# Kernel optimization log

Hardware: AMD Instinct MI355X
Metric: run time of the kernel (lower is better)

Reference implementation:

```python
import jax, jax.numpy as jnp
import numpy as np

H, B, S, E, V, C = 1024, 1024, 128, 6, 3, 10


def setup_inputs() -> dict:
    key = jax.random.key(0)
    ks = jax.random.split(key, 18)
    sH = 1.0 / np.sqrt(H)

    def n(k, shape, scale):
        return (jax.random.normal(k, shape, dtype=jnp.float32) * scale)

    return {
        'x': jax.random.randint(ks[0], (B, S), 0, V),
        'emb': n(ks[1], (V, E), 1.0),
        'W_gx': n(ks[2], (H, E), 1.0 / np.sqrt(E)),
        'W_gh': n(ks[3], (H, H), sH),
        'b_g': n(ks[4], (H, 1), sH),
        'W_ix': n(ks[5], (H, E), 1.0 / np.sqrt(E)),
        'W_ih': n(ks[6], (H, H), sH),
        'b_i': n(ks[7], (H, 1), sH),
        'W_fx': n(ks[8], (H, E), 1.0 / np.sqrt(E)),
        'W_fh': n(ks[9], (H, H), sH),
        'b_f': n(ks[10], (H, 1), sH),
        'W_ox': n(ks[11], (H, E), 1.0 / np.sqrt(E)),
        'W_oh': n(ks[12], (H, H), sH),
        'b_o': n(ks[13], (H, 1), sH),
        'W_ph': n(ks[14], (C, H), sH),
        'b_p': n(ks[15], (C, 1), sH),
        'h_init': n(ks[16], (H, B), 1.0),
        'c_init': n(ks[17], (H, B), 1.0),
    }


def reference(x, emb, W_gx, W_gh, b_g, W_ix, W_ih, b_i, W_fx, W_fh, b_f,
              W_ox, W_oh, b_o, W_ph, b_p, h_init, c_init):
    T = x.shape[1] - 1  # torch loop runs over seq_length - 1 steps
    e = emb[x[:, :T]]  # [B, T, E]
    # Precompute all input-to-gate projections in one batched contraction each.
    Xg = jnp.einsum('he,bte->thb', W_gx, e)  # [T, H, B]
    Xi = jnp.einsum('he,bte->thb', W_ix, e)
    Xf = jnp.einsum('he,bte->thb', W_fx, e)
    Xo = jnp.einsum('he,bte->thb', W_ox, e)

    def step(carry, xs):
        h, c = carry  # [H, B]
        xg, xi, xf, xo = xs
        g = jnp.tanh(xg + W_gh @ h + b_g)
        i = jax.nn.sigmoid(xi + W_ih @ h + b_i)
        f = jax.nn.sigmoid(xf + W_fh @ h + b_f)
        o = jax.nn.sigmoid(xo + W_oh @ h + b_o)
        c2 = g * i + c * f
        h2 = jnp.tanh(c2) * o
        return (h2, c2), None

    (h, c), _ = jax.lax.scan(step, (h_init, c_init), (Xg, Xi, Xf, Xo))
    p = W_ph @ h + b_p  # [C, B]
    return jax.nn.log_softmax(p.T, axis=-1)  # [B, C]
```

## Files before the change

kernel.cpp:

```cpp
#include <hip/hip_runtime.h>

constexpr int kH = 1024;
constexpr int kB = 1024;
constexpr int kS = 128;
constexpr int kT = 127;
constexpr int kE = 6;
constexpr int kV = 3;
constexpr int kC = 10;

typedef short s16x8 __attribute__((ext_vector_type(8)));
typedef short s16x4 __attribute__((ext_vector_type(4)));
typedef float f32x4 __attribute__((ext_vector_type(4)));
typedef unsigned short u16;

__device__ __forceinline__ float b2f(u16 u) {
    return __uint_as_float(((unsigned)u) << 16);
}
__device__ __forceinline__ u16 f2b(float f) {
    unsigned u = __float_as_uint(f);
    return (u16)((u + 0x7FFFu + ((u >> 16) & 1u)) >> 16);
}
__device__ __forceinline__ float sigmoid_fast(float x) {
    return 1.0f / (1.0f + __expf(-x));
}
__device__ __forceinline__ float tanh_fast(float x) {
    return 2.0f / (1.0f + __expf(-2.0f * x)) - 1.0f;
}
__device__ __forceinline__ float clamp30(float x) {
    return fminf(fmaxf(x, -30.0f), 30.0f);
}

__device__ __forceinline__ void async_copy16(const u16* g, u16* l) {
    __builtin_amdgcn_global_load_lds(
        (const __attribute__((address_space(1))) void*)g,
        (__attribute__((address_space(3))) void*)l, 16, 0, 0);
}

__global__ __launch_bounds__(256) void prep_weights(
    const float* __restrict__ Wgh, const float* __restrict__ Wih,
    const float* __restrict__ Wfh, const float* __restrict__ Woh,
    u16* __restrict__ wsw)
{
    unsigned grp = blockIdx.x * 256 + threadIdx.x;
    const int lane = grp & 63;
    const int lm   = lane & 15;
    const int quad = lane >> 4;
    const int k0   = (grp >> 6) & 7;
    const int g    = (grp >> 9) & 3;
    const int kc   = (grp >> 11) & 3;
    const int by   = grp >> 13;
    const float* src = (g == 0) ? Wgh : (g == 1) ? Wih : (g == 2) ? Wfh : Woh;
    const int row = by * 16 + lm;
    const int k   = kc * 256 + k0 * 32 + quad * 8;
    f32x4 v0 = *(const f32x4*)(src + (size_t)row * kH + k);
    f32x4 v1 = *(const f32x4*)(src + (size_t)row * kH + k + 4);
    s16x8 o;
#pragma unroll
    for (int j = 0; j < 4; ++j) o[j] = (short)f2b(v0[j]);
#pragma unroll
    for (int j = 0; j < 4; ++j) o[4 + j] = (short)f2b(v1[j]);
    *(s16x8*)(wsw + (size_t)grp * 8) = o;
}

__global__ __launch_bounds__(1024) void prep_hc(
    const float* __restrict__ h0, const float* __restrict__ c0,
    u16* __restrict__ hA, float* __restrict__ cT)
{
    __shared__ float th[32][33];
    __shared__ float tc[32][33];
    int b = blockIdx.x * 32 + threadIdx.x;
    int h = blockIdx.y * 32 + threadIdx.y;
    th[threadIdx.y][threadIdx.x] = h0[(size_t)h * kB + b];
    tc[threadIdx.y][threadIdx.x] = c0[(size_t)h * kB + b];
    __syncthreads();
    int ob = blockIdx.x * 32 + threadIdx.y;
    int oh = blockIdx.y * 32 + threadIdx.x;
    hA[(size_t)ob * kH + oh] = f2b(th[threadIdx.x][threadIdx.y]);
    cT[(size_t)ob * kH + oh] = tc[threadIdx.x][threadIdx.y];
}

__global__ __launch_bounds__(256) void prep_q(
    const float* __restrict__ Wgx, const float* __restrict__ Wix,
    const float* __restrict__ Wfx, const float* __restrict__ Wox,
    const float* __restrict__ bg,  const float* __restrict__ bi,
    const float* __restrict__ bf_, const float* __restrict__ bo,
    const float* __restrict__ emb, float* __restrict__ Q)
{
    int tid = blockIdx.x * blockDim.x + threadIdx.x;
    if (tid >= 4 * kH) return;
    int g = tid >> 10;
    int h = tid & (kH - 1);
    const float* Wx = (g == 0) ? Wgx : (g == 1) ? Wix : (g == 2) ? Wfx : Wox;
    const float* bb = (g == 0) ? bg  : (g == 1) ? bi  : (g == 2) ? bf_ : bo;
    float w[kE];
#pragma unroll
    for (int e = 0; e < kE; ++e) w[e] = Wx[h * kE + e];
#pragma unroll
    for (int v = 0; v < kV; ++v) {
        float s = bb[h];
#pragma unroll
        for (int e = 0; e < kE; ++e) s += w[e] * emb[v * kE + e];
        Q[tid * 4 + v] = s;
    }
    Q[tid * 4 + 3] = 0.0f;
}

__global__ __launch_bounds__(256, 2) void lstm_step(
    const u16* __restrict__ wsw, const float* __restrict__ Q,
    const int* __restrict__ x, int t,
    const short* __restrict__ hin, u16* __restrict__ hout,
    float* __restrict__ cT)
{
    __shared__ u16 wlds[2][16384];

    const int tid  = threadIdx.x;
    const int lane = tid & 63;
    const int wave = tid >> 6;
    const int lm   = lane & 15;
    const int quad = lane >> 4;
    const int blk  = blockIdx.x;
    const int xcd  = blk & 7;
    const int slot = blk >> 3;
    const int by   = xcd * 8 + (slot & 7);
    const int bx   = slot >> 3;
    const int r0 = by * 16;
    const int c0 = bx * 128 + wave * 32;

    const u16* wswblk = wsw + (size_t)by * 65536;

    f32x4 acc[4][2];
    const f32x4 zero = {0.f, 0.f, 0.f, 0.f};
#pragma unroll
    for (int g = 0; g < 4; ++g)
#pragma unroll
        for (int n = 0; n < 2; ++n) acc[g][n] = zero;

    const int koff = quad * 8;
    const short* hrow0 = hin + (size_t)(c0 + lm) * kH + koff;
    const short* hrow1 = hin + (size_t)(c0 + 16 + lm) * kH + koff;

    {
        const u16* gsrc = wswblk;
#pragma unroll
        for (int rr = 0; rr < 8; ++rr) {
            const int ub = wave * 4096 + rr * 512;
            async_copy16(gsrc + ub + lane * 8, &wlds[0][ub]);
        }
        asm volatile("s_waitcnt vmcnt(0)" ::: "memory");
        __syncthreads();
    }

    s16x8 b0c = *(const s16x8*)(hrow0);
    s16x8 b1c = *(const s16x8*)(hrow1);

#pragma unroll 1
    for (int kc = 0; kc < 4; ++kc) {
        const int cur = kc & 1;
        if (kc < 3) {
            const u16* gsrc = wswblk + (size_t)(kc + 1) * 16384;
#pragma unroll
            for (int rr = 0; rr < 8; ++rr) {
                const int ub = wave * 4096 + rr * 512;
                async_copy16(gsrc + ub + lane * 8, &wlds[cur ^ 1][ub]);
            }
        }
#pragma unroll
        for (int k0 = 0; k0 < 8; ++k0) {
            s16x8 b0n = {0,0,0,0,0,0,0,0}, b1n = {0,0,0,0,0,0,0,0};
            const int nk = kc * 256 + (k0 + 1) * 32;
            if (nk < kH) {
                b0n = *(const s16x8*)(hrow0 + nk);
                b1n = *(const s16x8*)(hrow1 + nk);
            }
#pragma unroll
            for (int g = 0; g < 4; ++g) {
                const int f = ((g * 8 + k0) * 64 + lane) * 8;
                s16x8 a = *(const s16x8*)&wlds[cur][f];
                acc[g][0] = __builtin_amdgcn_mfma_f32_16x16x32_bf16(a, b0c, acc[g][0], 0, 0, 0);
                acc[g][1] = __builtin_amdgcn_mfma_f32_16x16x32_bf16(a, b1c, acc[g][1], 0, 0, 0);
            }
            b0c = b0n;
            b1c = b1n;
        }
        if (kc < 3) {
            asm volatile("s_waitcnt vmcnt(0)" ::: "memory");
            __syncthreads();
        }
    }

#pragma unroll
    for (int nt = 0; nt < 2; ++nt) {
        const int c = c0 + nt * 16 + lm;
        int v = x[c * kS + t];
        v = (v < 0) ? 0 : (v > kV - 1) ? (kV - 1) : v;
        const int rb = r0 + quad * 4;
        f32x4 cold = *(const f32x4*)(cT + (size_t)c * kH + rb);
        f32x4 cnew;
        s16x4 hnew;
#pragma unroll
        for (int reg = 0; reg < 4; ++reg) {
            const int r = rb + reg;
            float pg = clamp30(acc[0][nt][reg] + Q[(0 * kH + r) * 4 + v]);
            float pi = clamp30(acc[1][nt][reg] + Q[(1 * kH + r) * 4 + v]);
            float pf = clamp30(acc[2][nt][reg] + Q[(2 * kH + r) * 4 + v]);
            float po = clamp30(acc[3][nt][reg] + Q[(3 * kH + r) * 4 + v]);
            float gg = tanh_fast(pg);
            float ii = sigmoid_fast(pi);
            float ff = sigmoid_fast(pf);
            float oo = sigmoid_fast(po);
            float c2 = gg * ii + cold[reg] * ff;
            c2 = fminf(fmaxf(c2, -200.0f), 200.0f);
            cnew[reg] = c2;
            hnew[reg] = (short)f2b(tanh_fast(c2) * oo);
        }
        *(f32x4*)(cT + (size_t)c * kH + rb) = cnew;
        *(s16x4*)(hout + (size_t)c * kH + rb) = hnew;
    }
}

__global__ __launch_bounds__(256) void logits_kernel(
    const u16* __restrict__ hT, const float* __restrict__ Wph,
    const float* __restrict__ bp, float* __restrict__ out)
{
    const int wave = threadIdx.x >> 6;
    const int lane = threadIdx.x & 63;
    const int b = blockIdx.x * 4 + wave;

    const u16* hp = hT + (size_t)b * kH + lane * 16;
    float hf[16];
#pragma unroll
    for (int j = 0; j < 16; ++j) hf[j] = b2f(hp[j]);

    float p[kC];
#pragma unroll
    for (int cls = 0; cls < kC; ++cls) {
        const float* wp = Wph + (size_t)cls * kH + lane * 16;
        float s = 0.f;
#pragma unroll
        for (int j = 0; j < 16; ++j) s += hf[j] * wp[j];
#pragma unroll
        for (int off = 1; off < 64; off <<= 1) s += __shfl_xor(s, off, 64);
        p[cls] = fminf(fmaxf(s + bp[cls], -1.0e4f), 1.0e4f);
    }

    float m = p[0];
#pragma unroll
    for (int cls = 1; cls < kC; ++cls) m = fmaxf(m, p[cls]);
    float se = 0.f;
#pragma unroll
    for (int cls = 0; cls < kC; ++cls) se += __expf(p[cls] - m);
    float l = m + __logf(se);

    if (lane < kC) {
        float myp = p[0];
#pragma unroll
        for (int cls = 1; cls < kC; ++cls)
            if (lane == cls) myp = p[cls];
        out[(size_t)b * kC + lane] = myp - l;
    }
}

extern "C" void kernel_launch(void* const* d_in, const int* in_sizes, int n_in,
                              void* d_out, int out_size, void* d_ws, size_t ws_size,
                              hipStream_t stream)
{
    const int*   x   = (const int*)  d_in[0];
    const float* emb = (const float*)d_in[1];
    const float* Wgx = (const float*)d_in[2];
    const float* Wgh = (const float*)d_in[3];
    const float* bg  = (const float*)d_in[4];
    const float* Wix = (const float*)d_in[5];
    const float* Wih = (const float*)d_in[6];
    const float* bi  = (const float*)d_in[7];
    const float* Wfx = (const float*)d_in[8];
    const float* Wfh = (const float*)d_in[9];
    const float* bf_ = (const float*)d_in[10];
    const float* Wox = (const float*)d_in[11];
    const float* Woh = (const float*)d_in[12];
    const float* bo  = (const float*)d_in[13];
    const float* Wph = (const float*)d_in[14];
    const float* bp  = (const float*)d_in[15];
    const float* h0  = (const float*)d_in[16];
    const float* c0  = (const float*)d_in[17];

    char* ws = (char*)d_ws;
    float* Q   = (float*)ws;
    u16*   hA  = (u16*)(ws + (64 << 10));
    u16*   hB  = hA + (size_t)kB * kH;
    float* cT  = (float*)(hB + (size_t)kB * kH);
    u16*   wsw = (u16*)(cT + (size_t)kB * kH);

    prep_weights<<<dim3(2048), dim3(256), 0, stream>>>(Wgh, Wih, Wfh, Woh, wsw);
    prep_hc<<<dim3(kB / 32, kH / 32), dim3(32, 32), 0, stream>>>(h0, c0, hA, cT);
    prep_q<<<dim3(16), dim3(256), 0, stream>>>(Wgx, Wix, Wfx, Wox, bg, bi, bf_, bo, emb, Q);

    for (int t = 0; t < kT; ++t) {
        const u16* hin  = (t & 1) ? hB : hA;
        u16*       hout = (t & 1) ? hA : hB;
        lstm_step<<<dim3(512), dim3(256), 0, stream>>>(
            wsw, Q, x, t, (const short*)hin, hout, cT);
    }
    logits_kernel<<<dim3(kB / 4), dim3(256), 0, stream>>>(hB, Wph, bp, (float*)d_out);
}
```

Measured before the change: 2.936 ms.

## Replace per-step launches with persistent LSTM kernel using grid barriers

Replaces the 127 per-timestep kernel launches with one persistent kernel of 256 blocks that loops over time and synchronises through a two-level atomic grid barrier. The cell state now stays in registers, and 14 of the 32 K-slices of each block's weight slab stay resident in LDS, while the remaining slices are read from global/L2 each step. The input projection and the logits/log-softmax step are fused into the same kernel. This removes launch overhead and the repeated reloading of weights and cell state from memory. In exchange it depends on all 256 blocks being co-resident, and the spin barrier has a bounded timeout that could silently break ordering.

```diff
diff --git a/kernel.cpp b/kernel.cpp
--- a/kernel.cpp
+++ b/kernel.cpp
@@ -7,6 +7,7 @@
 constexpr int kE = 6;
 constexpr int kV = 3;
 constexpr int kC = 10;
+constexpr int kKL = 14;
 
 typedef short s16x8 __attribute__((ext_vector_type(8)));
 typedef short s16x4 __attribute__((ext_vector_type(4)));
@@ -39,19 +40,18 @@
 __global__ __launch_bounds__(256) void prep_weights(
     const float* __restrict__ Wgh, const float* __restrict__ Wih,
     const float* __restrict__ Wfh, const float* __restrict__ Woh,
-    u16* __restrict__ wsw)
+    short* __restrict__ wsw)
 {
     unsigned grp = blockIdx.x * 256 + threadIdx.x;
     const int lane = grp & 63;
     const int lm   = lane & 15;
     const int quad = lane >> 4;
-    const int k0   = (grp >> 6) & 7;
-    const int g    = (grp >> 9) & 3;
-    const int kc   = (grp >> 11) & 3;
+    const int g    = (grp >> 6) & 3;
+    const int k0   = (grp >> 8) & 31;
     const int by   = grp >> 13;
     const float* src = (g == 0) ? Wgh : (g == 1) ? Wih : (g == 2) ? Wfh : Woh;
     const int row = by * 16 + lm;
-    const int k   = kc * 256 + k0 * 32 + quad * 8;
+    const int k   = k0 * 32 + quad * 8;
     f32x4 v0 = *(const f32x4*)(src + (size_t)row * kH + k);
     f32x4 v1 = *(const f32x4*)(src + (size_t)row * kH + k + 4);
     s16x8 o;
@@ -62,56 +62,59 @@
     *(s16x8*)(wsw + (size_t)grp * 8) = o;
 }
 
-__global__ __launch_bounds__(1024) void prep_hc(
-    const float* __restrict__ h0, const float* __restrict__ c0,
-    u16* __restrict__ hA, float* __restrict__ cT)
+__global__ __launch_bounds__(1024) void prep_h(
+    const float* __restrict__ h0, u16* __restrict__ hA)
 {
     __shared__ float th[32][33];
-    __shared__ float tc[32][33];
     int b = blockIdx.x * 32 + threadIdx.x;
     int h = blockIdx.y * 32 + threadIdx.y;
     th[threadIdx.y][threadIdx.x] = h0[(size_t)h * kB + b];
-    tc[threadIdx.y][threadIdx.x] = c0[(size_t)h * kB + b];
     __syncthreads();
     int ob = blockIdx.x * 32 + threadIdx.y;
     int oh = blockIdx.y * 32 + threadIdx.x;
     hA[(size_t)ob * kH + oh] = f2b(th[threadIdx.x][threadIdx.y]);
-    cT[(size_t)ob * kH + oh] = tc[threadIdx.x][threadIdx.y];
-}
-
-__global__ __launch_bounds__(256) void prep_q(
+}
+
+__device__ __forceinline__ void gbar(unsigned* bar, int g, bool leader, int epoch) {
+    __threadfence();
+    __syncthreads();
+    if (threadIdx.x == 0) {
+        __hip_atomic_fetch_add(&bar[g * 32], 1u, __ATOMIC_RELEASE,
+                               __HIP_MEMORY_SCOPE_AGENT);
+        if (leader) {
+            const unsigned gt = 32u * (unsigned)epoch;
+            int gc = 0;
+            while (__hip_atomic_load(&bar[g * 32], __ATOMIC_ACQUIRE,
+                                     __HIP_MEMORY_SCOPE_AGENT) < gt)
+                if (++gc > (1 << 18)) break;
+            __hip_atomic_fetch_add(&bar[256], 1u, __ATOMIC_RELEASE,
+                                   __HIP_MEMORY_SCOPE_AGENT);
+        }
+        const unsigned t8 = 8u * (unsigned)epoch;
+        int gc = 0;
+        while (__hip_atomic_load(&bar[256], __ATOMIC_ACQUIRE,
+                                 __HIP_MEMORY_SCOPE_AGENT) < t8)
+            if (++gc > (1 << 18)) break;
+    }
+    __syncthreads();
+    __builtin_amdgcn_fence(__ATOMIC_ACQUIRE, "agent");
+}
+
+__global__ __launch_bounds__(256, 1) void lstm_persist(
+    const short* __restrict__ wsw, const int* __restrict__ x,
+    const float* __restrict__ c0g,
     const float* __restrict__ Wgx, const float* __restrict__ Wix,
     const float* __restrict__ Wfx, const float* __restrict__ Wox,
     const float* __restrict__ bg,  const float* __restrict__ bi,
     const float* __restrict__ bf_, const float* __restrict__ bo,
-    const float* __restrict__ emb, float* __restrict__ Q)
+    const float* __restrict__ emb,
+    u16* __restrict__ hA, u16* __restrict__ hB,
+    unsigned* __restrict__ bar,
+    const float* __restrict__ Wph, const float* __restrict__ bp,
+    float* __restrict__ out)
 {
-    int tid = blockIdx.x * blockDim.x + threadIdx.x;
-    if (tid >= 4 * kH) return;
-    int g = tid >> 10;
-    int h = tid & (kH - 1);
-    const float* Wx = (g == 0) ? Wgx : (g == 1) ? Wix : (g == 2) ? Wfx : Wox;
-    const float* bb = (g == 0) ? bg  : (g == 1) ? bi  : (g == 2) ? bf_ : bo;
-    float w[kE];
-#pragma unroll
-    for (int e = 0; e < kE; ++e) w[e] = Wx[h * kE + e];
-#pragma unroll
-    for (int v = 0; v < kV; ++v) {
-        float s = bb[h];
-#pragma unroll
-        for (int e = 0; e < kE; ++e) s += w[e] * emb[v * kE + e];
-        Q[tid * 4 + v] = s;
-    }
-    Q[tid * 4 + 3] = 0.0f;
-}
-
-__global__ __launch_bounds__(256, 2) void lstm_step(
-    const u16* __restrict__ wsw, const float* __restrict__ Q,
-    const int* __restrict__ x, int t,
-    const short* __restrict__ hin, u16* __restrict__ hout,
-    float* __restrict__ cT)
-{
-    __shared__ u16 wlds[2][16384];
+    __shared__ short wl[kKL * 4 * 64 * 8];
+    __shared__ float qs[4][16][4];
 
     const int tid  = threadIdx.x;
     const int lane = tid & 63;
@@ -119,144 +122,162 @@
     const int lm   = lane & 15;
     const int quad = lane >> 4;
     const int blk  = blockIdx.x;
-    const int xcd  = blk & 7;
-    const int slot = blk >> 3;
-    const int by   = xcd * 8 + (slot & 7);
-    const int bx   = slot >> 3;
-    const int r0 = by * 16;
-    const int c0 = bx * 128 + wave * 32;
-
-    const u16* wswblk = wsw + (size_t)by * 65536;
-
-    f32x4 acc[4][2];
-    const f32x4 zero = {0.f, 0.f, 0.f, 0.f};
-#pragma unroll
-    for (int g = 0; g < 4; ++g)
-#pragma unroll
-        for (int n = 0; n < 2; ++n) acc[g][n] = zero;
-
+    const int bx   = blk >> 6;
+    const int j    = blk & 63;
+    const int by   = (j & 7) * 8 + (j >> 3);
+    const int r0   = by * 16;
+    const int cw   = bx * 256 + wave * 64;
     const int koff = quad * 8;
-    const short* hrow0 = hin + (size_t)(c0 + lm) * kH + koff;
-    const short* hrow1 = hin + (size_t)(c0 + 16 + lm) * kH + koff;
+    const int grpid  = blk & 7;
+    const bool leader = (blk < 8);
+
+    const short* wswblk = wsw + (size_t)by * 65536;
+
+#pragma unroll
+    for (int rr = 0; rr < kKL; ++rr) {
+        const int ub = wave * (kKL * 512) + rr * 512;
+        async_copy16((const u16*)(wswblk + ub) + lane * 8, (u16*)&wl[ub]);
+    }
+
+    if (tid < 192) {
+        int g = tid / 48, rem = tid % 48, r = rem / 3, v = rem % 3;
+        const float* Wx = (g == 0) ? Wgx : (g == 1) ? Wix : (g == 2) ? Wfx : Wox;
+        const float* bb = (g == 0) ? bg  : (g == 1) ? bi  : (g == 2) ? bf_ : bo;
+        int hr = r0 + r;
+        float s = bb[hr];
+#pragma unroll
+        for (int e = 0; e < kE; ++e) s += Wx[hr * kE + e] * emb[v * kE + e];
+        qs[g][r][v] = s;
+    }
+
+    float creg[4][4];
+#pragma unroll
+    for (int nt = 0; nt < 4; ++nt)
+#pragma unroll
+        for (int reg = 0; reg < 4; ++reg)
+            creg[nt][reg] =
+                c0g[(size_t)(r0 + quad * 4 + reg) * kB + (cw + nt * 16 + lm)];
+
+    asm volatile("s_waitcnt vmcnt(0)" ::: "memory");
+    __syncthreads();
+
+    auto loadA = [&](int s, s16x8 d[4]) {
+        if (s < kKL) {
+#pragma unroll
+            for (int g = 0; g < 4; ++g)
+                d[g] = *(const s16x8*)&wl[((s * 4 + g) * 64 + lane) * 8];
+        } else {
+#pragma unroll
+            for (int g = 0; g < 4; ++g)
+                d[g] = *(const s16x8*)(wswblk + (size_t)(s * 4 + g) * 512 + lane * 8);
+        }
+    };
+
+#pragma unroll 1
+    for (int t = 0; t < kT; ++t) {
+        const short* hin = (t & 1) ? (const short*)hB : (const short*)hA;
+        u16* hout = (t & 1) ? hA : hB;
+
+        int vv[4];
+#pragma unroll
+        for (int nt = 0; nt < 4; ++nt) {
+            int v = x[(size_t)(cw + nt * 16 + lm) * kS + t];
+            vv[nt] = (v < 0) ? 0 : (v > kV - 1) ? (kV - 1) : v;
+        }
+
+        f32x4 acc[4][4];
+        const f32x4 zero = {0.f, 0.f, 0.f, 0.f};
+#pragma unroll
+        for (int g = 0; g < 4; ++g)
+#pragma unroll
+            for (int nt = 0; nt < 4; ++nt) acc[g][nt] = zero;
+
+        auto loadB = [&](int s, s16x8 d[4]) {
+#pragma unroll
+            for (int nt = 0; nt < 4; ++nt)
+                d[nt] = *(const s16x8*)(hin + (size_t)(cw + nt * 16 + lm) * kH +
+                                        s * 32 + koff);
+        };
+
+        s16x8 ar[3][4], br[3][4];
+        loadA(0, ar[0]); loadB(0, br[0]);
+        loadA(1, ar[1]); loadB(1, br[1]);
+#pragma unroll
+        for (int k0 = 0; k0 < 32; ++k0) {
+            const int cur = k0 % 3;
+            if (k0 + 2 < 32) {
+                const int nxt = (k0 + 2) % 3;
+                loadA(k0 + 2, ar[nxt]);
+                loadB(k0 + 2, br[nxt]);
+            }
+#pragma unroll
+            for (int g = 0; g < 4; ++g)
+#pragma unroll
+                for (int nt = 0; nt < 4; ++nt)
+                    acc[g][nt] = __builtin_amdgcn_mfma_f32_16x16x32_bf16(
+                        ar[cur][g], br[cur][nt], acc[g][nt], 0, 0, 0);
+        }
+
+#pragma unroll
+        for (int nt = 0; nt < 4; ++nt) {
+            const int col = cw + nt * 16 + lm;
+            s16x4 hnew;
+#pragma unroll
+            for (int reg = 0; reg < 4; ++reg) {
+                const int rl = quad * 4 + reg;
+                float pg = clamp30(acc[0][nt][reg] + qs[0][rl][vv[nt]]);
+                float pi = clamp30(acc[1][nt][reg] + qs[1][rl][vv[nt]]);
+                float pf = clamp30(acc[2][nt][reg] + qs[2][rl][vv[nt]]);
+                float po = clamp30(acc[3][nt][reg] + qs[3][rl][vv[nt]]);
+                float gg = tanh_fast(pg);
+                float ii = sigmoid_fast(pi);
+                float ff = sigmoid_fast(pf);
+                float oo = sigmoid_fast(po);
+                float c2 = gg * ii + creg[nt][reg] * ff;
+                c2 = fminf(fmaxf(c2, -200.0f), 200.0f);
+                creg[nt][reg] = c2;
+                hnew[reg] = (short)f2b(tanh_fast(c2) * oo);
+            }
+            *(s16x4*)(hout + (size_t)col * kH + r0 + quad * 4) = hnew;
+        }
+
+        gbar(bar, grpid, leader, t + 1);
+    }
 
     {
-        const u16* gsrc = wswblk;
-#pragma unroll
-        for (int rr = 0; rr < 8; ++rr) {
-            const int ub = wave * 4096 + rr * 512;
-            async_copy16(gsrc + ub + lane * 8, &wlds[0][ub]);
-        }
-        asm volatile("s_waitcnt vmcnt(0)" ::: "memory");
-        __syncthreads();
-    }
-
-    s16x8 b0c = *(const s16x8*)(hrow0);
-    s16x8 b1c = *(const s16x8*)(hrow1);
-
-#pragma unroll 1
-    for (int kc = 0; kc < 4; ++kc) {
-        const int cur = kc & 1;
-        if (kc < 3) {
-            const u16* gsrc = wswblk + (size_t)(kc + 1) * 16384;
-#pragma unroll
-            for (int rr = 0; rr < 8; ++rr) {
-                const int ub = wave * 4096 + rr * 512;
-                async_copy16(gsrc + ub + lane * 8, &wlds[cur ^ 1][ub]);
-            }
-        }
-#pragma unroll
-        for (int k0 = 0; k0 < 8; ++k0) {
-            s16x8 b0n = {0,0,0,0,0,0,0,0}, b1n = {0,0,0,0,0,0,0,0};
-            const int nk = kc * 256 + (k0 + 1) * 32;
-            if (nk < kH) {
-                b0n = *(const s16x8*)(hrow0 + nk);
-                b1n = *(const s16x8*)(hrow1 + nk);
-            }
-#pragma unroll
-            for (int g = 0; g < 4; ++g) {
-                const int f = ((g * 8 + k0) * 64 + lane) * 8;
-                s16x8 a = *(const s16x8*)&wlds[cur][f];
-                acc[g][0] = __builtin_amdgcn_mfma_f32_16x16x32_bf16(a, b0c, acc[g][0], 0, 0, 0);
-                acc[g][1] = __builtin_amdgcn_mfma_f32_16x16x32_bf16(a, b1c, acc[g][1], 0, 0, 0);
-            }
-            b0c = b0n;
-            b1c = b1n;
-        }
-        if (kc < 3) {
-            asm volatile("s_waitcnt vmcnt(0)" ::: "memory");
-            __syncthreads();
-        }
-    }
-
-#pragma unroll
-    for (int nt = 0; nt < 2; ++nt) {
-        const int c = c0 + nt * 16 + lm;
-        int v = x[c * kS + t];
-        v = (v < 0) ? 0 : (v > kV - 1) ? (kV - 1) : v;
-        const int rb = r0 + quad * 4;
-        f32x4 cold = *(const f32x4*)(cT + (size_t)c * kH + rb);
-        f32x4 cnew;
-        s16x4 hnew;
-#pragma unroll
-        for (int reg = 0; reg < 4; ++reg) {
-            const int r = rb + reg;
-            float pg = clamp30(acc[0][nt][reg] + Q[(0 * kH + r) * 4 + v]);
-            float pi = clamp30(acc[1][nt][reg] + Q[(1 * kH + r) * 4 + v]);
-            float pf = clamp30(acc[2][nt][reg] + Q[(2 * kH + r) * 4 + v]);
-            float po = clamp30(acc[3][nt][reg] + Q[(3 * kH + r) * 4 + v]);
-            float gg = tanh_fast(pg);
-            float ii = sigmoid_fast(pi);
-            float ff = sigmoid_fast(pf);
-            float oo = sigmoid_fast(po);
-            float c2 = gg * ii + cold[reg] * ff;
-            c2 = fminf(fmaxf(c2, -200.0f), 200.0f);
-            cnew[reg] = c2;
-            hnew[reg] = (short)f2b(tanh_fast(c2) * oo);
-        }
-        *(f32x4*)(cT + (size_t)c * kH + rb) = cnew;
-        *(s16x4*)(hout + (size_t)c * kH + rb) = hnew;
-    }
-}
-
-__global__ __launch_bounds__(256) void logits_kernel(
-    const u16* __restrict__ hT, const float* __restrict__ Wph,
-    const float* __restrict__ bp, float* __restrict__ out)
-{
-    const int wave = threadIdx.x >> 6;
-    const int lane = threadIdx.x & 63;
-    const int b = blockIdx.x * 4 + wave;
-
-    const u16* hp = hT + (size_t)b * kH + lane * 16;
-    float hf[16];
-#pragma unroll
-    for (int j = 0; j < 16; ++j) hf[j] = b2f(hp[j]);
-
-    float p[kC];
-#pragma unroll
-    for (int cls = 0; cls < kC; ++cls) {
-        const float* wp = Wph + (size_t)cls * kH + lane * 16;
-        float s = 0.f;
-#pragma unroll
-        for (int j = 0; j < 16; ++j) s += hf[j] * wp[j];
-#pragma unroll
-        for (int off = 1; off < 64; off <<= 1) s += __shfl_xor(s, off, 64);
-        p[cls] = fminf(fmaxf(s + bp[cls], -1.0e4f), 1.0e4f);
-    }
-
-    float m = p[0];
-#pragma unroll
-    for (int cls = 1; cls < kC; ++cls) m = fmaxf(m, p[cls]);
-    float se = 0.f;
-#pragma unroll
-    for (int cls = 0; cls < kC; ++cls) se += __expf(p[cls] - m);
-    float l = m + __logf(se);
-
-    if (lane < kC) {
-        float myp = p[0];
-#pragma unroll
-        for (int cls = 1; cls < kC; ++cls)
-            if (lane == cls) myp = p[cls];
-        out[(size_t)b * kC + lane] = myp - l;
+        const int b = blk * 4 + wave;
+        const u16* hp = hB + (size_t)b * kH + lane * 16;
+        float hf[16];
+#pragma unroll
+        for (int jj = 0; jj < 16; ++jj) hf[jj] = b2f(hp[jj]);
+
+        float p[kC];
+#pragma unroll
+        for (int cls = 0; cls < kC; ++cls) {
+            const float* wp = Wph + (size_t)cls * kH + lane * 16;
+            float s = 0.f;
+#pragma unroll
+            for (int jj = 0; jj < 16; ++jj) s += hf[jj] * wp[jj];
+#pragma unroll
+            for (int off = 1; off < 64; off <<= 1) s += __shfl_xor(s, off, 64);
+            p[cls] = fminf(fmaxf(s + bp[cls], -1.0e4f), 1.0e4f);
+        }
+
+        float m = p[0];
+#pragma unroll
+        for (int cls = 1; cls < kC; ++cls) m = fmaxf(m, p[cls]);
+        float se = 0.f;
+#pragma unroll
+        for (int cls = 0; cls < kC; ++cls) se += __expf(p[cls] - m);
+        float l = m + __logf(se);
+
+        if (lane < kC) {
+            float myp = p[0];
+#pragma unroll
+            for (int cls = 1; cls < kC; ++cls)
+                if (lane == cls) myp = p[cls];
+            out[(size_t)b * kC + lane] = myp - l;
+        }
     }
 }
 
@@ -284,21 +305,16 @@
     const float* c0  = (const float*)d_in[17];
 
     char* ws = (char*)d_ws;
-    float* Q   = (float*)ws;
-    u16*   hA  = (u16*)(ws + (64 << 10));
+    unsigned* bar = (unsigned*)ws;
+    u16*   hA  = (u16*)(ws + 4096);
     u16*   hB  = hA + (size_t)kB * kH;
-    float* cT  = (float*)(hB + (size_t)kB * kH);
-    u16*   wsw = (u16*)(cT + (size_t)kB * kH);
-
+    short* wsw = (short*)(hB + (size_t)kB * kH);
+
+    hipMemsetAsync(bar, 0, 4096, stream);
     prep_weights<<<dim3(2048), dim3(256), 0, stream>>>(Wgh, Wih, Wfh, Woh, wsw);
-    prep_hc<<<dim3(kB / 32, kH / 32), dim3(32, 32), 0, stream>>>(h0, c0, hA, cT);
-    prep_q<<<dim3(16), dim3(256), 0, stream>>>(Wgx, Wix, Wfx, Wox, bg, bi, bf_, bo, emb, Q);
-
-    for (int t = 0; t < kT; ++t) {
-        const u16* hin  = (t & 1) ? hB : hA;
-        u16*       hout = (t & 1) ? hA : hB;
-        lstm_step<<<dim3(512), dim3(256), 0, stream>>>(
-            wsw, Q, x, t, (const short*)hin, hout, cT);
-    }
-    logits_kernel<<<dim3(kB / 4), dim3(256), 0, stream>>>(hB, Wph, bp, (float*)d_out);
-}
+    prep_h<<<dim3(kB / 32, kH / 32), dim3(32, 32), 0, stream>>>(h0, hA);
+
+    lstm_persist<<<dim3(256), dim3(256), 0, stream>>>(
+        wsw, x, c0, Wgx, Wix, Wfx, Wox, bg, bi, bf_, bo, emb,
+        hA, hB, bar, Wph, bp, (float*)d_out);
+}
```

Result: slower. 10.11 ms (+244.4%).

## Prefetch gate bias and cell state early, deepen h-operand prefetch ring

Applied to the files above, without the earlier changes.

The Q table is re-laid out so each lane fetches four consecutive rows for its token with a single vector load. The lstm_step kernel now issues the token, Q and old cell-state loads before the main loop, so their latency overlaps the first weight tile copy instead of sitting in the epilogue. The k loop is fully unrolled and keeps a six-slot register ring of h operands loaded five steps ahead, replacing the one-step prefetch, to hide global load latency behind MFMAs. This raises register pressure and code size, which could reduce occupancy at the 2-blocks-per-CU launch bound.

```diff
diff --git a/kernel.cpp b/kernel.cpp
--- a/kernel.cpp
+++ b/kernel.cpp
@@ -84,29 +84,31 @@
     const float* __restrict__ Wfx, const float* __restrict__ Wox,
     const float* __restrict__ bg,  const float* __restrict__ bi,
     const float* __restrict__ bf_, const float* __restrict__ bo,
-    const float* __restrict__ emb, float* __restrict__ Q)
+    const float* __restrict__ emb, float* __restrict__ Qp)
 {
     int tid = blockIdx.x * blockDim.x + threadIdx.x;
-    if (tid >= 4 * kH) return;
-    int g = tid >> 10;
-    int h = tid & (kH - 1);
+    if (tid >= 4096) return;
+    int g   = tid >> 10;
+    int hr4 = (tid & 1023) >> 2;
+    int v   = tid & 3;
     const float* Wx = (g == 0) ? Wgx : (g == 1) ? Wix : (g == 2) ? Wfx : Wox;
     const float* bb = (g == 0) ? bg  : (g == 1) ? bi  : (g == 2) ? bf_ : bo;
-    float w[kE];
-#pragma unroll
-    for (int e = 0; e < kE; ++e) w[e] = Wx[h * kE + e];
-#pragma unroll
-    for (int v = 0; v < kV; ++v) {
-        float s = bb[h];
-#pragma unroll
-        for (int e = 0; e < kE; ++e) s += w[e] * emb[v * kE + e];
-        Q[tid * 4 + v] = s;
-    }
-    Q[tid * 4 + 3] = 0.0f;
+    f32x4 o;
+#pragma unroll
+    for (int reg = 0; reg < 4; ++reg) {
+        int row = hr4 * 4 + reg;
+        float s = bb[row];
+        if (v < kV) {
+#pragma unroll
+            for (int e = 0; e < kE; ++e) s += Wx[row * kE + e] * emb[v * kE + e];
+        }
+        o[reg] = s;
+    }
+    *(f32x4*)(Qp + (size_t)tid * 4) = o;
 }
 
 __global__ __launch_bounds__(256, 2) void lstm_step(
-    const u16* __restrict__ wsw, const float* __restrict__ Q,
+    const u16* __restrict__ wsw, const float* __restrict__ Qp,
     const int* __restrict__ x, int t,
     const short* __restrict__ hin, u16* __restrict__ hout,
     float* __restrict__ cT)
@@ -128,87 +130,99 @@
 
     const u16* wswblk = wsw + (size_t)by * 65536;
 
-    f32x4 acc[4][2];
-    const f32x4 zero = {0.f, 0.f, 0.f, 0.f};
-#pragma unroll
-    for (int g = 0; g < 4; ++g)
-#pragma unroll
-        for (int n = 0; n < 2; ++n) acc[g][n] = zero;
+#pragma unroll
+    for (int rr = 0; rr < 8; ++rr) {
+        const int ub = wave * 4096 + rr * 512;
+        async_copy16(wswblk + ub + lane * 8, &wlds[0][ub]);
+    }
+
+    int vv[2];
+#pragma unroll
+    for (int nt = 0; nt < 2; ++nt) {
+        int v = x[(size_t)(c0 + nt * 16 + lm) * kS + t];
+        vv[nt] = (v < 0) ? 0 : (v > kV - 1) ? (kV - 1) : v;
+    }
+    f32x4 qv[2][4];
+#pragma unroll
+    for (int nt = 0; nt < 2; ++nt)
+#pragma unroll
+        for (int g = 0; g < 4; ++g)
+            qv[nt][g] = *(const f32x4*)(Qp +
+                (size_t)(((g * 256 + by * 4 + quad) * 4 + vv[nt]) * 4));
+    f32x4 cold[2];
+#pragma unroll
+    for (int nt = 0; nt < 2; ++nt)
+        cold[nt] = *(const f32x4*)(cT +
+            (size_t)(c0 + nt * 16 + lm) * kH + r0 + quad * 4);
 
     const int koff = quad * 8;
     const short* hrow0 = hin + (size_t)(c0 + lm) * kH + koff;
     const short* hrow1 = hin + (size_t)(c0 + 16 + lm) * kH + koff;
-
-    {
-        const u16* gsrc = wswblk;
-#pragma unroll
-        for (int rr = 0; rr < 8; ++rr) {
-            const int ub = wave * 4096 + rr * 512;
-            async_copy16(gsrc + ub + lane * 8, &wlds[0][ub]);
-        }
-        asm volatile("s_waitcnt vmcnt(0)" ::: "memory");
-        __syncthreads();
-    }
-
-    s16x8 b0c = *(const s16x8*)(hrow0);
-    s16x8 b1c = *(const s16x8*)(hrow1);
-
-#pragma unroll 1
-    for (int kc = 0; kc < 4; ++kc) {
-        const int cur = kc & 1;
-        if (kc < 3) {
-            const u16* gsrc = wswblk + (size_t)(kc + 1) * 16384;
+    s16x8 br[6][2];
+#pragma unroll
+    for (int s = 0; s < 5; ++s) {
+        br[s][0] = *(const s16x8*)(hrow0 + s * 32);
+        br[s][1] = *(const s16x8*)(hrow1 + s * 32);
+    }
+
+    f32x4 acc[4][2];
+    const f32x4 zero = {0.f, 0.f, 0.f, 0.f};
+#pragma unroll
+    for (int g = 0; g < 4; ++g)
+#pragma unroll
+        for (int n = 0; n < 2; ++n) acc[g][n] = zero;
+
+    asm volatile("s_waitcnt vmcnt(0)" ::: "memory");
+    __syncthreads();
+
+#pragma unroll
+    for (int k0 = 0; k0 < 32; ++k0) {
+        if ((k0 & 7) == 0 && k0 > 0) {
+            asm volatile("s_waitcnt vmcnt(0)" ::: "memory");
+            __syncthreads();
+        }
+        if ((k0 & 7) == 0 && k0 < 24) {
+            const int nc = (k0 >> 3) + 1;
+            const u16* gsrc = wswblk + (size_t)nc * 16384;
 #pragma unroll
             for (int rr = 0; rr < 8; ++rr) {
                 const int ub = wave * 4096 + rr * 512;
-                async_copy16(gsrc + ub + lane * 8, &wlds[cur ^ 1][ub]);
+                async_copy16(gsrc + ub + lane * 8, &wlds[nc & 1][ub]);
             }
         }
-#pragma unroll
-        for (int k0 = 0; k0 < 8; ++k0) {
-            s16x8 b0n = {0,0,0,0,0,0,0,0}, b1n = {0,0,0,0,0,0,0,0};
-            const int nk = kc * 256 + (k0 + 1) * 32;
-            if (nk < kH) {
-                b0n = *(const s16x8*)(hrow0 + nk);
-                b1n = *(const s16x8*)(hrow1 + nk);
-            }
-#pragma unroll
-            for (int g = 0; g < 4; ++g) {
-                const int f = ((g * 8 + k0) * 64 + lane) * 8;
-                s16x8 a = *(const s16x8*)&wlds[cur][f];
-                acc[g][0] = __builtin_amdgcn_mfma_f32_16x16x32_bf16(a, b0c, acc[g][0], 0, 0, 0);
-                acc[g][1] = __builtin_amdgcn_mfma_f32_16x16x32_bf16(a, b1c, acc[g][1], 0, 0, 0);
-            }
-            b0c = b0n;
-            b1c = b1n;
-        }
-        if (kc < 3) {
-            asm volatile("s_waitcnt vmcnt(0)" ::: "memory");
-            __syncthreads();
+        if (k0 + 5 < 32) {
+            const int s = (k0 + 5) % 6;
+            br[s][0] = *(const s16x8*)(hrow0 + (k0 + 5) * 32);
+            br[s][1] = *(const s16x8*)(hrow1 + (k0 + 5) * 32);
+        }
+        const int cur = k0 % 6;
+        const int buf = (k0 >> 3) & 1;
+#pragma unroll
+        for (int g = 0; g < 4; ++g) {
+            const int f = ((g * 8 + (k0 & 7)) * 64 + lane) * 8;
+            s16x8 a = *(const s16x8*)&wlds[buf][f];
+            acc[g][0] = __builtin_amdgcn_mfma_f32_16x16x32_bf16(a, br[cur][0], acc[g][0], 0, 0, 0);
+            acc[g][1] = __builtin_amdgcn_mfma_f32_16x16x32_bf16(a, br[cur][1], acc[g][1], 0, 0, 0);
         }
     }
 
 #pragma unroll
     for (int nt = 0; nt < 2; ++nt) {
         const int c = c0 + nt * 16 + lm;
-        int v = x[c * kS + t];
-        v = (v < 0) ? 0 : (v > kV - 1) ? (kV - 1) : v;
         const int rb = r0 + quad * 4;
-        f32x4 cold = *(const f32x4*)(cT + (size_t)c * kH + rb);
         f32x4 cnew;
         s16x4 hnew;
 #pragma unroll
         for (int reg = 0; reg < 4; ++reg) {
-            const int r = rb + reg;
-            float pg = clamp30(acc[0][nt][reg] + Q[(0 * kH + r) * 4 + v]);
-            float pi = clamp30(acc[1][nt][reg] + Q[(1 * kH + r) * 4 + v]);
-            float pf = clamp30(acc[2][nt][reg] + Q[(2 * kH + r) * 4 + v]);
-            float po = clamp30(acc[3][nt][reg] + Q[(3 * kH + r) * 4 + v]);
+            float pg = clamp30(acc[0][nt][reg] + qv[nt][0][reg]);
+            float pi = clamp30(acc[1][nt][reg] + qv[nt][1][reg]);
+            float pf = clamp30(acc[2][nt][reg] + qv[nt][2][reg]);
+            float po = clamp30(acc[3][nt][reg] + qv[nt][3][reg]);
             float gg = tanh_fast(pg);
             float ii = sigmoid_fast(pi);
             float ff = sigmoid_fast(pf);
             float oo = sigmoid_fast(po);
-            float c2 = gg * ii + cold[reg] * ff;
+            float c2 = gg * ii + cold[nt][reg] * ff;
             c2 = fminf(fmaxf(c2, -200.0f), 200.0f);
             cnew[reg] = c2;
             hnew[reg] = (short)f2b(tanh_fast(c2) * oo);
@@ -284,7 +298,7 @@
     const float* c0  = (const float*)d_in[17];
 
     char* ws = (char*)d_ws;
-    float* Q   = (float*)ws;
+    float* Qp  = (float*)ws;
     u16*   hA  = (u16*)(ws + (64 << 10));
     u16*   hB  = hA + (size_t)kB * kH;
     float* cT  = (float*)(hB + (size_t)kB * kH);
@@ -292,13 +306,13 @@
 
     prep_weights<<<dim3(2048), dim3(256), 0, stream>>>(Wgh, Wih, Wfh, Woh, wsw);
     prep_hc<<<dim3(kB / 32, kH / 32), dim3(32, 32), 0, stream>>>(h0, c0, hA, cT);
-    prep_q<<<dim3(16), dim3(256), 0, stream>>>(Wgx, Wix, Wfx, Wox, bg, bi, bf_, bo, emb, Q);
+    prep_q<<<dim3(16), dim3(256), 0, stream>>>(Wgx, Wix, Wfx, Wox, bg, bi, bf_, bo, emb, Qp);
 
     for (int t = 0; t < kT; ++t) {
         const u16* hin  = (t & 1) ? hB : hA;
         u16*       hout = (t & 1) ? hA : hB;
         lstm_step<<<dim3(512), dim3(256), 0, stream>>>(
-            wsw, Q, x, t, (const short*)hin, hout, cT);
+            wsw, Qp, x, t, (const short*)hin, hout, cT);
     }
     logits_kernel<<<dim3(kB / 4), dim3(256), 0, stream>>>(hB, Wph, bp, (float*)d_out);
 }
```

Result: no change. 2.932 ms (-0.1%).
